# Kernel optimization log

Measured on AMD Instinct MI355X. Metric: run time of the kernel, lower is better.

## Reference

```python
import jax, jax.numpy as jnp
import numpy as np

N, D_IN, D_OUT, L, R = 32768, 2048, 2048, 8, 16
LORA_ALPHA, LORA_RANK = 32.0, 16.0
SCALE = LORA_ALPHA / LORA_RANK  # applied because alpha != rank


def setup_inputs() -> dict:
    key = jax.random.key(0)
    ks = jax.random.split(key, 6)
    x = jax.random.normal(ks[0], (N, D_IN), dtype=jnp.float32)
    W = jax.random.normal(ks[1], (D_OUT, D_IN), dtype=jnp.float32) * 0.02
    b = jax.random.normal(ks[2], (D_OUT,), dtype=jnp.float32) * 0.02
    A_all = jax.random.normal(ks[3], (L, R, D_IN), dtype=jnp.float32) * 0.02
    B_all = jax.random.normal(ks[4], (L, D_OUT, R), dtype=jnp.float32) * 0.02
    # per-sample adapter index; -1 would mean "no LoRA" (handled by mask below)
    lora_idx = jax.random.randint(ks[5], (N,), 0, L, dtype=jnp.int32)
    return {"x": x, "W": W, "b": b, "A_all": A_all, "B_all": B_all, "lora_idx": lora_idx}


def reference(x, W, b, A_all, B_all, lora_idx):
    # Base linear: base_layer(x) -> x @ W.T + b
    base_out = x @ W.T + b  # [N, D_OUT]
    # Multi-LoRA: per-token adapter selection. Instead of Python grouping
    # (gather-matmul-scatter per group), compute the tiny down-projection for
    # all adapters and mask-select, then one fused up-projection.
    u = jnp.einsum('nd,lrd->nlr', x, A_all)  # [N, L, R] (small: r=16)
    Lnum = A_all.shape[0]
    sel = (lora_idx[:, None] == jnp.arange(Lnum, dtype=lora_idx.dtype)[None, :]) \
          & (lora_idx >= 0)[:, None]  # [N, L] one-hot, zero row if idx < 0
    u = u * sel[:, :, None].astype(u.dtype) * jnp.asarray(SCALE, u.dtype)
    # delta[n] = scale * (x[n] @ A[idx_n].T) @ B[idx_n].T, zeros elsewhere
    delta = jnp.einsum('nlr,lor->no', u, B_all)  # [N, D_OUT]
    return base_out + delta
```

## Files before the change

### kernel.cpp

```cpp
#include <hip/hip_runtime.h>
#include <stdint.h>

#define N_TOK 32768
#define DIN   2048
#define DOUT  2048
#define LAD   8
#define RRK   16
#define KCAT  2176
#define SCALE 2.0f

typedef __attribute__((ext_vector_type(8))) short bf16x8;
typedef __attribute__((ext_vector_type(4))) float f32x4;

__device__ __forceinline__ unsigned short f2bf(float f) {
    union { float f; unsigned u; } c; c.f = f;
    return (unsigned short)((c.u + 0x7FFFu + ((c.u >> 16) & 1u)) >> 16);
}

__device__ __forceinline__ uint4 pack8(float4 a, float4 b) {
    union { unsigned short s[8]; uint4 v; } u;
    u.s[0] = f2bf(a.x); u.s[1] = f2bf(a.y); u.s[2] = f2bf(a.z); u.s[3] = f2bf(a.w);
    u.s[4] = f2bf(b.x); u.s[5] = f2bf(b.y); u.s[6] = f2bf(b.z); u.s[7] = f2bf(b.w);
    return u.v;
}

__device__ __forceinline__ void async16(const void* g, void* l) {
    __builtin_amdgcn_global_load_lds(
        (const __attribute__((address_space(1))) void*)g,
        (__attribute__((address_space(3))) void*)l, 16, 0, 0);
}


__global__ __launch_bounds__(256) void prep_w(const float* __restrict__ W,
                                              const float* __restrict__ A_all,
                                              const float* __restrict__ B_all,
                                              unsigned short* __restrict__ wcat,
                                              unsigned short* __restrict__ acat) {
    const int NW = DOUT * DIN / 8;
    const int NB = DOUT * LAD;
    const int NA = LAD * RRK * DIN / 8;
    int tid = blockIdx.x * 256 + threadIdx.x;
    if (tid < NW) {
        int e = tid * 8;
        int o = e / DIN, k = e % DIN;
        float4 f0 = *(const float4*)(W + e);
        float4 f1 = *(const float4*)(W + e + 4);
        *(uint4*)(wcat + (size_t)o * KCAT + k) = pack8(f0, f1);
    } else if (tid < NW + NB) {
        int t = tid - NW;
        int o = t >> 3, l = t & 7;
        const float* src = B_all + ((size_t)l * DOUT + o) * RRK;
        float4 f0 = *(const float4*)(src + 0);
        float4 f1 = *(const float4*)(src + 4);
        float4 f2 = *(const float4*)(src + 8);
        float4 f3 = *(const float4*)(src + 12);
        unsigned short* dst = wcat + (size_t)o * KCAT + DIN + l * RRK;
        *(uint4*)(dst + 0) = pack8(f0, f1);
        *(uint4*)(dst + 8) = pack8(f2, f3);
    } else if (tid < NW + NB + NA) {
        int e = (tid - NW - NB) * 8;
        float4 f0 = *(const float4*)(A_all + e);
        float4 f1 = *(const float4*)(A_all + e + 4);
        *(uint4*)(acat + e) = pack8(f0, f1);
    }
}

__global__ __launch_bounds__(256) void conv_x(const float* __restrict__ x,
                                              unsigned short* __restrict__ xcat) {
    size_t e = ((size_t)blockIdx.x * 256 + threadIdx.x) * 8;
    int n = (int)(e / DIN), k = (int)(e % DIN);
    float4 f0 = *(const float4*)(x + e);
    float4 f1 = *(const float4*)(x + e + 4);
    *(uint4*)(xcat + (size_t)n * KCAT + k) = pack8(f0, f1);
}

__global__ __launch_bounds__(256) void u_gemm(const unsigned short* __restrict__ xcat,
                                              const unsigned short* __restrict__ acat,
                                              const int* __restrict__ lidx,
                                              unsigned short* __restrict__ xcat_w) {
    __shared__ short As[128 * 32];
    __shared__ short Bs[128 * 32];
    const int tid = threadIdx.x;
    const int lane = tid & 63, wv = tid >> 6;
    const int wm = wv >> 1, wn = wv & 1;
    const int quad = lane >> 4, lm = lane & 15;
    const int row0 = blockIdx.x * 128;
    const int sg = (lane & 3) ^ ((lane >> 3) & 3);
    const int swg = quad ^ ((lm >> 1) & 3);

    f32x4 acc[4][4];
    f32x4 zero = {0.f, 0.f, 0.f, 0.f};
#pragma unroll
    for (int i = 0; i < 4; ++i)
#pragma unroll
        for (int j = 0; j < 4; ++j) acc[i][j] = zero;

    for (int kt = 0; kt < DIN / 32; ++kt) {
        const unsigned short* ga = xcat + (size_t)row0 * KCAT + kt * 32;
        const unsigned short* gb = acat + kt * 32;
        __syncthreads();
#pragma unroll
        for (int it = 0; it < 2; ++it) {
            int cw = it * 4 + wv;
            int r = (cw * 64 + lane) >> 2;
            async16(ga + (size_t)r * KCAT + sg * 8, (void*)(As + cw * 512));
            async16(gb + (size_t)r * DIN + sg * 8, (void*)(Bs + cw * 512));
        }
        __syncthreads();
        bf16x8 a[4], b[4];
#pragma unroll
        for (int mi = 0; mi < 4; ++mi)
            a[mi] = *(const bf16x8*)&As[(wm * 64 + mi * 16 + lm) * 32 + swg * 8];
#pragma unroll
        for (int ni = 0; ni < 4; ++ni)
            b[ni] = *(const bf16x8*)&Bs[(wn * 64 + ni * 16 + lm) * 32 + swg * 8];
#pragma unroll
        for (int mi = 0; mi < 4; ++mi)
#pragma unroll
            for (int ni = 0; ni < 4; ++ni)
                acc[mi][ni] = __builtin_amdgcn_mfma_f32_16x16x32_bf16(a[mi], b[ni], acc[mi][ni], 0, 0, 0);
    }

#pragma unroll
    for (int mi = 0; mi < 4; ++mi) {
#pragma unroll
        for (int e = 0; e < 4; ++e) {
            int t = row0 + wm * 64 + mi * 16 + quad * 4 + e;
            int l = lidx[t];
#pragma unroll
            for (int ni = 0; ni < 4; ++ni) {
                int j = wn * 64 + ni * 16 + lm;
                float v = ((j >> 4) == l) ? acc[mi][ni][e] * SCALE : 0.0f;
                xcat_w[(size_t)t * KCAT + DIN + j] = f2bf(v);
            }
        }
    }
}

__global__ __launch_bounds__(256) void gemm_main(const unsigned short* __restrict__ xcat,
                                                 const unsigned short* __restrict__ wcat,
                                                 const float* __restrict__ bias,
                                                 float* __restrict__ out) {
    __shared__ short As[128 * 32];
    __shared__ short Bs[128 * 32];
    const int tid = threadIdx.x;
    const int lane = tid & 63, wv = tid >> 6;
    const int wm = wv >> 1, wn = wv & 1;
    const int quad = lane >> 4, lm = lane & 15;
    const int col0 = blockIdx.x * 128;
    const int row0 = blockIdx.y * 128;
    const int sg = (lane & 3) ^ ((lane >> 3) & 3);
    const int swg = quad ^ ((lm >> 1) & 3);

    f32x4 acc[4][4];
    f32x4 zero = {0.f, 0.f, 0.f, 0.f};
#pragma unroll
    for (int i = 0; i < 4; ++i)
#pragma unroll
        for (int j = 0; j < 4; ++j) acc[i][j] = zero;

    for (int kt = 0; kt < KCAT / 32; ++kt) {
        const unsigned short* ga = xcat + (size_t)row0 * KCAT + kt * 32;
        const unsigned short* gb = wcat + (size_t)col0 * KCAT + kt * 32;
        __syncthreads();
#pragma unroll
        for (int it = 0; it < 2; ++it) {
            int cw = it * 4 + wv;
            int r = (cw * 64 + lane) >> 2;
            async16(ga + (size_t)r * KCAT + sg * 8, (void*)(As + cw * 512));
            async16(gb + (size_t)r * KCAT + sg * 8, (void*)(Bs + cw * 512));
        }
        __syncthreads();
        bf16x8 a[4], b[4];
#pragma unroll
        for (int mi = 0; mi < 4; ++mi)
            a[mi] = *(const bf16x8*)&As[(wm * 64 + mi * 16 + lm) * 32 + swg * 8];
#pragma unroll
        for (int ni = 0; ni < 4; ++ni)
            b[ni] = *(const bf16x8*)&Bs[(wn * 64 + ni * 16 + lm) * 32 + swg * 8];
#pragma unroll
        for (int mi = 0; mi < 4; ++mi)
#pragma unroll
            for (int ni = 0; ni < 4; ++ni)
                acc[mi][ni] = __builtin_amdgcn_mfma_f32_16x16x32_bf16(a[mi], b[ni], acc[mi][ni], 0, 0, 0);
    }

#pragma unroll
    for (int ni = 0; ni < 4; ++ni) {
        int col = col0 + wn * 64 + ni * 16 + lm;
        float bv = bias[col];
#pragma unroll
        for (int mi = 0; mi < 4; ++mi) {
            int rbase = row0 + wm * 64 + mi * 16 + quad * 4;
#pragma unroll
            for (int e = 0; e < 4; ++e)
                out[(size_t)(rbase + e) * DOUT + col] = acc[mi][ni][e] + bv;
        }
    }
}

extern "C" void kernel_launch(void* const* d_in, const int* in_sizes, int n_in,
                              void* d_out, int out_size, void* d_ws, size_t ws_size,
                              hipStream_t stream) {
    const float* x     = (const float*)d_in[0];
    const float* W     = (const float*)d_in[1];
    const float* bias  = (const float*)d_in[2];
    const float* A_all = (const float*)d_in[3];
    const float* B_all = (const float*)d_in[4];
    const int*   lidx  = (const int*)d_in[5];
    float* out = (float*)d_out;

    char* ws = (char*)d_ws;
    unsigned short* xcat = (unsigned short*)ws;
    unsigned short* wcat = (unsigned short*)(ws + (size_t)N_TOK * KCAT * 2);
    unsigned short* acat = (unsigned short*)(ws + (size_t)N_TOK * KCAT * 2
                                                + (size_t)DOUT * KCAT * 2);

    prep_w<<<2240, 256, 0, stream>>>(W, A_all, B_all, wcat, acat);
    conv_x<<<(N_TOK * (DIN / 8)) / 256, 256, 0, stream>>>(x, xcat);
    u_gemm<<<N_TOK / 128, 256, 0, stream>>>(xcat, acat, lidx, xcat);
    gemm_main<<<dim3(DOUT / 128, N_TOK / 128), 256, 0, stream>>>(xcat, wcat, bias, out);
}
```

Before: 856.0 us.

## Pipeline main GEMM with 4-stage async LDS buffering and 256x256 tiles

Rewrites the main GEMM to use 256x256 output tiles with 512 threads, each wave computing 128x64. A four-buffer ring of async global-to-LDS loads keeps three k-tiles in flight, using vmcnt waits and a single barrier per iteration instead of two syncthreads. Block indices are remapped so neighbouring blocks share panels for better L2 reuse. LDS grows to 128KB per block and accumulator registers double, which may limit occupancy and relies on hand-counted vmcnt values being correct.

```diff
diff --git a/kernel.cpp b/kernel.cpp
--- a/kernel.cpp
+++ b/kernel.cpp
@@ -137,61 +137,99 @@
     }
 }
 
-__global__ __launch_bounds__(256) void gemm_main(const unsigned short* __restrict__ xcat,
-                                                 const unsigned short* __restrict__ wcat,
-                                                 const float* __restrict__ bias,
-                                                 float* __restrict__ out) {
-    __shared__ short As[128 * 32];
-    __shared__ short Bs[128 * 32];
+#define BKT 32
+#define NKT (KCAT / BKT)
+
+__global__ __launch_bounds__(512, 2) void gemm_main(const unsigned short* __restrict__ xcat,
+                                                    const unsigned short* __restrict__ wcat,
+                                                    const float* __restrict__ bias,
+                                                    float* __restrict__ out) {
+    __shared__ short As[4][256 * BKT];
+    __shared__ short Bs[4][256 * BKT];
     const int tid = threadIdx.x;
     const int lane = tid & 63, wv = tid >> 6;
-    const int wm = wv >> 1, wn = wv & 1;
+    const int wm = wv >> 2, wn = wv & 3;
     const int quad = lane >> 4, lm = lane & 15;
-    const int col0 = blockIdx.x * 128;
-    const int row0 = blockIdx.y * 128;
-    const int sg = (lane & 3) ^ ((lane >> 3) & 3);
+
+    const int orig = blockIdx.x;
+    const int swz = (orig & 7) * ((int)gridDim.x >> 3) + (orig >> 3);
+    const int col0 = (swz & 7) * 256;
+    const int row0 = (swz >> 3) * 256;
+
+    const int sg  = (lane & 3) ^ ((lane >> 3) & 3);
     const int swg = quad ^ ((lm >> 1) & 3);
 
-    f32x4 acc[4][4];
+    const int r0 = (wv * 64 + lane) >> 2;
+    const int r1 = ((8 + wv) * 64 + lane) >> 2;
+    const unsigned short* gaBase = xcat + (size_t)row0 * KCAT + sg * 8;
+    const unsigned short* gbBase = wcat + (size_t)col0 * KCAT + sg * 8;
+
+    f32x4 acc[8][4];
     f32x4 zero = {0.f, 0.f, 0.f, 0.f};
 #pragma unroll
-    for (int i = 0; i < 4; ++i)
+    for (int i = 0; i < 8; ++i)
 #pragma unroll
         for (int j = 0; j < 4; ++j) acc[i][j] = zero;
 
-    for (int kt = 0; kt < KCAT / 32; ++kt) {
-        const unsigned short* ga = xcat + (size_t)row0 * KCAT + kt * 32;
-        const unsigned short* gb = wcat + (size_t)col0 * KCAT + kt * 32;
-        __syncthreads();
-#pragma unroll
-        for (int it = 0; it < 2; ++it) {
-            int cw = it * 4 + wv;
-            int r = (cw * 64 + lane) >> 2;
-            async16(ga + (size_t)r * KCAT + sg * 8, (void*)(As + cw * 512));
-            async16(gb + (size_t)r * KCAT + sg * 8, (void*)(Bs + cw * 512));
-        }
-        __syncthreads();
-        bf16x8 a[4], b[4];
-#pragma unroll
-        for (int mi = 0; mi < 4; ++mi)
-            a[mi] = *(const bf16x8*)&As[(wm * 64 + mi * 16 + lm) * 32 + swg * 8];
-#pragma unroll
-        for (int ni = 0; ni < 4; ++ni)
-            b[ni] = *(const bf16x8*)&Bs[(wn * 64 + ni * 16 + lm) * 32 + swg * 8];
-#pragma unroll
-        for (int mi = 0; mi < 4; ++mi)
+    auto stage = [&](int t) {
+        const int buf = t & 3;
+        const unsigned short* ga = gaBase + t * BKT;
+        const unsigned short* gb = gbBase + t * BKT;
+        short* la = &As[buf][wv * 512];
+        short* lb = &Bs[buf][wv * 512];
+        async16(ga + (size_t)r0 * KCAT, (void*)la);
+        async16(ga + (size_t)r1 * KCAT, (void*)(la + 4096));
+        async16(gb + (size_t)r0 * KCAT, (void*)lb);
+        async16(gb + (size_t)r1 * KCAT, (void*)(lb + 4096));
+    };
+
+    auto compute = [&](int t) {
+        const int buf = t & 3;
+        bf16x8 a[8], b[4];
+        const short* pa = &As[buf][(wm * 128 + lm) * BKT + swg * 8];
+        const short* pb = &Bs[buf][(wn * 64 + lm) * BKT + swg * 8];
+#pragma unroll
+        for (int mi = 0; mi < 8; ++mi) a[mi] = *(const bf16x8*)(pa + mi * 16 * BKT);
+#pragma unroll
+        for (int ni = 0; ni < 4; ++ni) b[ni] = *(const bf16x8*)(pb + ni * 16 * BKT);
+#pragma unroll
+        for (int mi = 0; mi < 8; ++mi)
 #pragma unroll
             for (int ni = 0; ni < 4; ++ni)
                 acc[mi][ni] = __builtin_amdgcn_mfma_f32_16x16x32_bf16(a[mi], b[ni], acc[mi][ni], 0, 0, 0);
-    }
+    };
+
+    stage(0); stage(1); stage(2);
+
+    for (int t = 0; t < NKT - 3; ++t) {
+        asm volatile("s_waitcnt vmcnt(8)" ::: "memory");
+        __builtin_amdgcn_s_barrier();
+        asm volatile("" ::: "memory");
+        stage(t + 3);
+        compute(t);
+    }
+    asm volatile("s_waitcnt vmcnt(8)" ::: "memory");
+    __builtin_amdgcn_s_barrier();
+    asm volatile("" ::: "memory");
+    compute(NKT - 3);
+
+    asm volatile("s_waitcnt vmcnt(4)" ::: "memory");
+    __builtin_amdgcn_s_barrier();
+    asm volatile("" ::: "memory");
+    compute(NKT - 2);
+
+    asm volatile("s_waitcnt vmcnt(0)" ::: "memory");
+    __builtin_amdgcn_s_barrier();
+    asm volatile("" ::: "memory");
+    compute(NKT - 1);
 
 #pragma unroll
     for (int ni = 0; ni < 4; ++ni) {
         int col = col0 + wn * 64 + ni * 16 + lm;
         float bv = bias[col];
 #pragma unroll
-        for (int mi = 0; mi < 4; ++mi) {
-            int rbase = row0 + wm * 64 + mi * 16 + quad * 4;
+        for (int mi = 0; mi < 8; ++mi) {
+            int rbase = row0 + wm * 128 + mi * 16 + quad * 4;
 #pragma unroll
             for (int e = 0; e < 4; ++e)
                 out[(size_t)(rbase + e) * DOUT + col] = acc[mi][ni][e] + bv;
@@ -219,5 +257,5 @@
     prep_w<<<2240, 256, 0, stream>>>(W, A_all, B_all, wcat, acat);
     conv_x<<<(N_TOK * (DIN / 8)) / 256, 256, 0, stream>>>(x, xcat);
     u_gemm<<<N_TOK / 128, 256, 0, stream>>>(xcat, acat, lidx, xcat);
-    gemm_main<<<dim3(DOUT / 128, N_TOK / 128), 256, 0, stream>>>(xcat, wcat, bias, out);
-}
+    gemm_main<<<dim3((N_TOK / 256) * (DOUT / 256)), 512, 0, stream>>>(xcat, wcat, bias, out);
+}
```

Result: slower. 915.3 us (+6.9%).

## Rewrite main GEMM as 256x256-tile double-buffered pipelined kernel with 8 waves

Applied to the files above, without the earlier changes.

Replaces the 128x128 single-stage main GEMM with a 256x256 tile, 512-thread kernel using BK=64, double-buffered LDS with async global-to-LDS loads interleaved between MFMA quarter-blocks, explicit waitcnt/barrier scheduling and s_setprio. A grid swizzle groups blocks for L2 reuse, and an XOR swizzle on LDS rows avoids bank conflicts. It aims to hide memory latency and raise arithmetic intensity on the dominant GEMM. The cost is 128KB of LDS per block and heavy register use for a 128-float accumulator per thread, which may limit occupancy, and the hand-written wait counts are fragile.

```diff
diff --git a/kernel.cpp b/kernel.cpp
--- a/kernel.cpp
+++ b/kernel.cpp
@@ -29,7 +29,6 @@
         (const __attribute__((address_space(1))) void*)g,
         (__attribute__((address_space(3))) void*)l, 16, 0, 0);
 }
-
 
 __global__ __launch_bounds__(256) void prep_w(const float* __restrict__ W,
                                               const float* __restrict__ A_all,
@@ -137,64 +136,143 @@
     }
 }
 
-__global__ __launch_bounds__(256) void gemm_main(const unsigned short* __restrict__ xcat,
-                                                 const unsigned short* __restrict__ wcat,
-                                                 const float* __restrict__ bias,
-                                                 float* __restrict__ out) {
-    __shared__ short As[128 * 32];
-    __shared__ short Bs[128 * 32];
+#define BK2  64
+#define NKT2 (KCAT / BK2)
+#define NIT  (NKT2 / 2)
+
+#define VMC4() asm volatile("s_waitcnt vmcnt(4)" ::: "memory")
+#define VMC0() asm volatile("s_waitcnt vmcnt(0)" ::: "memory")
+#define LGK8() asm volatile("s_waitcnt lgkmcnt(8)" ::: "memory")
+#define LGK0() asm volatile("s_waitcnt lgkmcnt(0)" ::: "memory")
+#define BARR() __builtin_amdgcn_s_barrier()
+#define SBR()  __builtin_amdgcn_sched_barrier(0)
+#define PRIO1() __builtin_amdgcn_s_setprio(1)
+#define PRIO0() __builtin_amdgcn_s_setprio(0)
+
+#define RD_A(D, QM)                                                            \
+    _Pragma("unroll") for (int mi = 0; mi < 4; ++mi)                           \
+    _Pragma("unroll") for (int ks = 0; ks < 2; ++ks) {                         \
+        const int rl = ((QM) * 4 + mi) * 16 + lm;                              \
+        const int ob = (rl * 128 + ks * 64 + quad * 16) ^ ((lm & 7) << 4);     \
+        aF[mi * 2 + ks] = *(const bf16x8*)((const char*)&lds[D][wm][0] + ob);  \
+    }
+
+#define RD_B(D, QN, BF)                                                        \
+    _Pragma("unroll") for (int ni = 0; ni < 2; ++ni)                           \
+    _Pragma("unroll") for (int ks = 0; ks < 2; ++ks) {                         \
+        const int rl = (wn & 1) * 64 + ((QN) * 2 + ni) * 16 + lm;              \
+        const int ob = (rl * 128 + ks * 64 + quad * 16) ^ ((lm & 7) << 4);     \
+        BF[ni * 2 + ks] =                                                      \
+            *(const bf16x8*)((const char*)&lds[D][2 + (wn >> 1)][0] + ob);     \
+    }
+
+#define MFMA16(QM, QN, BF)                                                     \
+    _Pragma("unroll") for (int mi = 0; mi < 4; ++mi)                           \
+    _Pragma("unroll") for (int ni = 0; ni < 2; ++ni)                           \
+    _Pragma("unroll") for (int ks = 0; ks < 2; ++ks)                           \
+        acc[(QM) * 4 + mi][(QN) * 2 + ni] =                                    \
+            __builtin_amdgcn_mfma_f32_16x16x32_bf16(                           \
+                aF[mi * 2 + ks], BF[ni * 2 + ks],                              \
+                acc[(QM) * 4 + mi][(QN) * 2 + ni], 0, 0, 0);
+
+__global__ __launch_bounds__(512, 2) void gemm_main(const unsigned short* __restrict__ xcat,
+                                                    const unsigned short* __restrict__ wcat,
+                                                    const float* __restrict__ bias,
+                                                    float* __restrict__ out) {
+    __shared__ short lds[2][4][8192];
     const int tid = threadIdx.x;
     const int lane = tid & 63, wv = tid >> 6;
-    const int wm = wv >> 1, wn = wv & 1;
+    const int wm = wv >> 2, wn = wv & 3;
     const int quad = lane >> 4, lm = lane & 15;
-    const int col0 = blockIdx.x * 128;
-    const int row0 = blockIdx.y * 128;
-    const int sg = (lane & 3) ^ ((lane >> 3) & 3);
-    const int swg = quad ^ ((lm >> 1) & 3);
-
-    f32x4 acc[4][4];
+
+    const int orig = blockIdx.x;
+    const int swz = (orig & 7) * ((int)gridDim.x >> 3) + (orig >> 3);
+    const int col0 = (swz & 7) * 256;
+    const int row0 = (swz >> 3) * 256;
+
+    const int rbase = wv * 8 + (lane >> 3);
+    const int csrc = ((((lane & 7) * 16) ^ (((lane >> 3) & 7) << 4)) >> 1);
+
+    auto stage = [&](int buf, int part, int gk) {
+        const int half = part & 1;
+        const unsigned short* g = (part < 2)
+            ? xcat + (size_t)(row0 + half * 128) * KCAT
+            : wcat + (size_t)(col0 + half * 128) * KCAT;
+        short* dbase = &lds[buf][part][0] + wv * 512;
+#pragma unroll
+        for (int j = 0; j < 2; ++j)
+            async16(g + (size_t)(j * 64 + rbase) * KCAT + gk * 64 + csrc,
+                    (void*)(dbase + j * 4096));
+    };
+
+    f32x4 acc[8][4];
     f32x4 zero = {0.f, 0.f, 0.f, 0.f};
 #pragma unroll
-    for (int i = 0; i < 4; ++i)
+    for (int i = 0; i < 8; ++i)
 #pragma unroll
         for (int j = 0; j < 4; ++j) acc[i][j] = zero;
 
-    for (int kt = 0; kt < KCAT / 32; ++kt) {
-        const unsigned short* ga = xcat + (size_t)row0 * KCAT + kt * 32;
-        const unsigned short* gb = wcat + (size_t)col0 * KCAT + kt * 32;
-        __syncthreads();
-#pragma unroll
-        for (int it = 0; it < 2; ++it) {
-            int cw = it * 4 + wv;
-            int r = (cw * 64 + lane) >> 2;
-            async16(ga + (size_t)r * KCAT + sg * 8, (void*)(As + cw * 512));
-            async16(gb + (size_t)r * KCAT + sg * 8, (void*)(Bs + cw * 512));
-        }
-        __syncthreads();
-        bf16x8 a[4], b[4];
-#pragma unroll
-        for (int mi = 0; mi < 4; ++mi)
-            a[mi] = *(const bf16x8*)&As[(wm * 64 + mi * 16 + lm) * 32 + swg * 8];
-#pragma unroll
-        for (int ni = 0; ni < 4; ++ni)
-            b[ni] = *(const bf16x8*)&Bs[(wn * 64 + ni * 16 + lm) * 32 + swg * 8];
-#pragma unroll
-        for (int mi = 0; mi < 4; ++mi)
-#pragma unroll
-            for (int ni = 0; ni < 4; ++ni)
-                acc[mi][ni] = __builtin_amdgcn_mfma_f32_16x16x32_bf16(a[mi], b[ni], acc[mi][ni], 0, 0, 0);
-    }
+    bf16x8 aF[8];
+    bf16x8 bF0[4], bF1[4];
+
+    stage(0, 0, 0); stage(0, 1, 0); stage(0, 2, 0); stage(0, 3, 0);
+    stage(1, 2, 1); stage(1, 3, 1);
+    VMC4();
+    BARR();
+
+    for (int it = 0; it < NIT - 1; ++it) {
+        RD_A(0, 0) RD_B(0, 0, bF0)
+        stage(1, 0, 2 * it + 1); LGK8();
+        BARR(); LGK0(); SBR(); PRIO1(); MFMA16(0, 0, bF0) PRIO0(); BARR();
+        RD_B(0, 1, bF1)
+        stage(1, 1, 2 * it + 1);
+        BARR(); LGK0(); SBR(); PRIO1(); MFMA16(0, 1, bF1) PRIO0(); BARR();
+        RD_A(0, 1)
+        stage(0, 2, 2 * it + 2);
+        BARR(); LGK0(); SBR(); PRIO1(); MFMA16(1, 1, bF1) PRIO0(); BARR();
+        stage(0, 3, 2 * it + 2);
+        BARR(); PRIO1(); MFMA16(1, 0, bF0) PRIO0(); VMC4(); BARR();
+
+        RD_A(1, 0) RD_B(1, 0, bF0)
+        stage(0, 0, 2 * it + 2); LGK8();
+        BARR(); LGK0(); SBR(); PRIO1(); MFMA16(0, 0, bF0) PRIO0(); BARR();
+        RD_B(1, 1, bF1)
+        stage(0, 1, 2 * it + 2);
+        BARR(); LGK0(); SBR(); PRIO1(); MFMA16(0, 1, bF1) PRIO0(); BARR();
+        RD_A(1, 1)
+        stage(1, 2, 2 * it + 3);
+        BARR(); LGK0(); SBR(); PRIO1(); MFMA16(1, 1, bF1) PRIO0(); BARR();
+        stage(1, 3, 2 * it + 3);
+        BARR(); PRIO1(); MFMA16(1, 0, bF0) PRIO0(); VMC4(); BARR();
+    }
+
+    RD_A(0, 0) RD_B(0, 0, bF0)
+    stage(1, 0, 2 * (NIT - 1) + 1); LGK8();
+    BARR(); LGK0(); SBR(); PRIO1(); MFMA16(0, 0, bF0) PRIO0(); BARR();
+    RD_B(0, 1, bF1)
+    stage(1, 1, 2 * (NIT - 1) + 1);
+    BARR(); LGK0(); SBR(); PRIO1(); MFMA16(0, 1, bF1) PRIO0(); BARR();
+    RD_A(0, 1)
+    BARR(); LGK0(); SBR(); PRIO1(); MFMA16(1, 1, bF1) PRIO0(); BARR();
+    BARR(); PRIO1(); MFMA16(1, 0, bF0) PRIO0(); VMC0(); BARR();
+    RD_A(1, 0) RD_B(1, 0, bF0)
+    BARR(); LGK0(); SBR(); PRIO1(); MFMA16(0, 0, bF0) PRIO0(); BARR();
+    RD_B(1, 1, bF1)
+    BARR(); LGK0(); SBR(); PRIO1(); MFMA16(0, 1, bF1) PRIO0(); BARR();
+    RD_A(1, 1)
+    BARR(); LGK0(); SBR(); PRIO1(); MFMA16(1, 1, bF1) PRIO0(); BARR();
+    PRIO1(); MFMA16(1, 0, bF0) PRIO0();
 
 #pragma unroll
     for (int ni = 0; ni < 4; ++ni) {
         int col = col0 + wn * 64 + ni * 16 + lm;
         float bv = bias[col];
 #pragma unroll
-        for (int mi = 0; mi < 4; ++mi) {
-            int rbase = row0 + wm * 64 + mi * 16 + quad * 4;
+        for (int mi = 0; mi < 8; ++mi) {
+            int rbase2 = row0 + wm * 128 + mi * 16 + quad * 4;
 #pragma unroll
             for (int e = 0; e < 4; ++e)
-                out[(size_t)(rbase + e) * DOUT + col] = acc[mi][ni][e] + bv;
+                out[(size_t)(rbase2 + e) * DOUT + col] = acc[mi][ni][e] + bv;
         }
     }
 }
@@ -219,5 +297,5 @@
     prep_w<<<2240, 256, 0, stream>>>(W, A_all, B_all, wcat, acat);
     conv_x<<<(N_TOK * (DIN / 8)) / 256, 256, 0, stream>>>(x, xcat);
     u_gemm<<<N_TOK / 128, 256, 0, stream>>>(xcat, acat, lidx, xcat);
-    gemm_main<<<dim3(DOUT / 128, N_TOK / 128), 256, 0, stream>>>(xcat, wcat, bias, out);
-}
+    gemm_main<<<dim3((N_TOK / 256) * (DOUT / 256)), 512, 0, stream>>>(xcat, wcat, bias, out);
+}
```

After: 788.9 us. 7.8% less time.
